# Optimization experiments

Measured on AMD Instinct MI355X. Metric: run time of the kernel, lower is better.

Reference implementation:

```python
import jax, jax.numpy as jnp
import numpy as np

N, D = 16384, 16     # nodes (hits), node feature dim (= embedding dim, slice is full)
K = 64               # max_num_neighbors
MAX_RADIUS = 6.0     # kNN radius cut
PID_MAX = 5000


def setup_inputs() -> dict:
    key = jax.random.key(0)
    k1, k2 = jax.random.split(key)
    x = jax.random.normal(k1, (N, D), dtype=jnp.float32)
    particle_id = jax.random.randint(k2, (N,), 0, PID_MAX, dtype=jnp.int32)
    return {"x": x, "particle_id": particle_id}


def reference(x, particle_id):
    # ml is None and embedding_slice=(None,None) -> embedding features are x itself
    emb = x
    # knn_graph: squared pairwise distances, self-loops excluded (diag = +inf)
    sq = jnp.sum(emb * emb, axis=1)                       # [N]
    d2 = sq[:, None] + sq[None, :] - 2.0 * (emb @ emb.T)  # [N, N]
    diag = jnp.arange(N)
    d2 = d2.at[diag, diag].set(jnp.inf)
    _, nbr = jax.lax.top_k(-d2, K)                        # [N, K] nearest neighbor ids
    src = nbr.reshape(-1)                                 # edge_index[0]: neighbor (source)
    dst = jnp.repeat(jnp.arange(N, dtype=src.dtype), K)   # edge_index[1]: query node
    # radius filter: keep edges with dist < max_radius (fixed shape -> boolean mask)
    diff = x[src] - x[dst]                                # [N*K, D]
    dists = jnp.sqrt(jnp.maximum(jnp.sum(diff * diff, axis=1), 0.0))
    mask = dists < MAX_RADIUS                             # [N*K]
    # edge truth labels: same (nonzero) particle id on both ends
    y = (particle_id[src] == particle_id[dst]) & (particle_id[src] > 0) & mask
    # edge features: [x_src - x_dst, x_src + x_dst], zeroed on masked-out edges
    edge_features = jnp.concatenate([diff, x[src] + x[dst]], axis=1)
    edge_features = edge_features * mask[:, None].astype(x.dtype)
    edge_index = jnp.stack([src, dst])                    # [2, N*K]
    return x, edge_index, y.astype(jnp.int32), edge_features, mask
```

## Files before the change

kernel.cpp:

```cpp
#include <hip/hip_runtime.h>

#define NN 16384
#define DD 16
#define KK 64
#define QQ 4
#define TPB 256
#define NQW 16
#define HIST 1024
#define HISTW (HIST/2)
#define LIST_MAX 768
#define CAND_MAX 256

__device__ __forceinline__ float halving_sumsq16(const float* v) {
    float p[16];
#pragma unroll
    for (int d = 0; d < 16; ++d) p[d] = __fmul_rn(v[d], v[d]);
    float r8[8];
#pragma unroll
    for (int j = 0; j < 8; ++j) r8[j] = __fadd_rn(p[j], p[j + 8]);
    float r4[4];
#pragma unroll
    for (int j = 0; j < 4; ++j) r4[j] = __fadd_rn(r8[j], r8[j + 4]);
    float r2[2];
#pragma unroll
    for (int j = 0; j < 2; ++j) r2[j] = __fadd_rn(r4[j], r4[j + 2]);
    return __fadd_rn(r2[0], r2[1]);
}

__device__ __forceinline__ float d2_of(const float* xi, const float* xj,
                                       float sqi, float sqj) {
    float dot = 0.0f;
#pragma unroll
    for (int d = 0; d < DD; ++d) dot = fmaf(xi[d], xj[d], dot);
    return __fsub_rn(__fadd_rn(sqi, sqj), __fmul_rn(2.0f, dot));
}

__device__ __forceinline__ int bucket_of(float d2) {
    int b = (int)__fmul_rn(d2, 4.0f);
    if (b < 0) b = 0;
    if (b >= HIST) b = HIST - 1;
    return b;
}

#define LOAD_XQ()                                                              \
    float xq[QQ][DD];                                                          \
    float sq[QQ], Tq[QQ];                                                      \
    _Pragma("unroll") for (int q = 0; q < QQ; ++q) {                           \
        const float4* p = reinterpret_cast<const float4*>(x + (iA + q) * DD);  \
        float4 a0 = p[0], a1 = p[1], a2 = p[2], a3 = p[3];                     \
        xq[q][0]=a0.x; xq[q][1]=a0.y; xq[q][2]=a0.z; xq[q][3]=a0.w;            \
        xq[q][4]=a1.x; xq[q][5]=a1.y; xq[q][6]=a1.z; xq[q][7]=a1.w;            \
        xq[q][8]=a2.x; xq[q][9]=a2.y; xq[q][10]=a2.z; xq[q][11]=a2.w;          \
        xq[q][12]=a3.x; xq[q][13]=a3.y; xq[q][14]=a3.z; xq[q][15]=a3.w;        \
        sq[q] = sqf[iA + q];                                                   \
        Tq[q] = 16.0f + sq[q] - 1.8f * sqrtf(32.0f + 4.0f * sq[q]);            \
    }

#define LOAD_XJ(j)                                                             \
    const float4* xj4 = reinterpret_cast<const float4*>(x + (j) * DD);         \
    float4 a0 = xj4[0], a1 = xj4[1], a2 = xj4[2], a3 = xj4[3];                 \
    float xj[DD] = {a0.x, a0.y, a0.z, a0.w, a1.x, a1.y, a1.z, a1.w,            \
                    a2.x, a2.y, a2.z, a2.w, a3.x, a3.y, a3.z, a3.w};

__global__ void prep_kernel(const float* __restrict__ x,
                            float* __restrict__ out_x,
                            float* __restrict__ sqf,
                            float* __restrict__ xt) {
    int i = blockIdx.x * blockDim.x + threadIdx.x;
    if (i < NN) {
        float v[DD];
#pragma unroll
        for (int d = 0; d < DD; ++d) v[d] = x[i * DD + d];
        sqf[i] = halving_sumsq16(v);
#pragma unroll
        for (int d = 0; d < DD; ++d) xt[d * NN + i] = v[d];
    }
    for (int t = i; t < NN * DD; t += gridDim.x * blockDim.x) {
        out_x[t] = x[t];
    }
}

__global__ __launch_bounds__(TPB, 6) void scan_kernel(
        const float* __restrict__ x,
        const float* __restrict__ xt,
        const float* __restrict__ sqf,
        unsigned int* __restrict__ ws_cnt,
        unsigned short* __restrict__ ws_list) {
    __shared__ unsigned short bm[NQW][TPB];
    __shared__ unsigned short list[QQ][LIST_MAX];
    __shared__ unsigned int wcnt[TPB / 64][QQ];
    __shared__ unsigned int s_listcnt[QQ];

    const int bid = blockIdx.x;
    const int tid = threadIdx.x;
    const int lane = tid & 63;
    const int w = tid >> 6;
    const int iA = bid * QQ;

    LOAD_XQ();

#pragma unroll 1
    for (int c = 0; c < NQW; ++c) {
        const int qd = c * TPB + tid;
        float4 sjv = reinterpret_cast<const float4*>(sqf)[qd];
        float4 acc[QQ];
#pragma unroll
        for (int q = 0; q < QQ; ++q) acc[q] = make_float4(0.f, 0.f, 0.f, 0.f);
#pragma unroll
        for (int d = 0; d < DD; ++d) {
            float4 xv = reinterpret_cast<const float4*>(xt + (long)d * NN)[qd];
#pragma unroll
            for (int q = 0; q < QQ; ++q) {
                acc[q].x = fmaf(xq[q][d], xv.x, acc[q].x);
                acc[q].y = fmaf(xq[q][d], xv.y, acc[q].y);
                acc[q].z = fmaf(xq[q][d], xv.z, acc[q].z);
                acc[q].w = fmaf(xq[q][d], xv.w, acc[q].w);
            }
        }
        unsigned int bits = 0;
#pragma unroll
        for (int q = 0; q < QQ; ++q) {
            float d2x = __fsub_rn(__fadd_rn(sq[q], sjv.x), __fmul_rn(2.0f, acc[q].x));
            float d2y = __fsub_rn(__fadd_rn(sq[q], sjv.y), __fmul_rn(2.0f, acc[q].y));
            float d2z = __fsub_rn(__fadd_rn(sq[q], sjv.z), __fmul_rn(2.0f, acc[q].z));
            float d2w = __fsub_rn(__fadd_rn(sq[q], sjv.w), __fmul_rn(2.0f, acc[q].w));
            if (d2x < Tq[q]) bits |= (1u << (0 * 4 + q));
            if (d2y < Tq[q]) bits |= (1u << (1 * 4 + q));
            if (d2z < Tq[q]) bits |= (1u << (2 * 4 + q));
            if (d2w < Tq[q]) bits |= (1u << (3 * 4 + q));
        }
        bm[c][tid] = (unsigned short)bits;
    }
    __syncthreads();

    {
        unsigned int cnt[QQ] = {0, 0, 0, 0};
#pragma unroll 1
        for (int c = 0; c < NQW; ++c) {
            unsigned int w16 = bm[c][tid];
#pragma unroll
            for (int q = 0; q < QQ; ++q)
                cnt[q] += (unsigned int)__popc(w16 & (0x1111u << q));
        }
        unsigned int excl[QQ];
#pragma unroll
        for (int q = 0; q < QQ; ++q) {
            unsigned int v = cnt[q];
#pragma unroll
            for (int off = 1; off < 64; off <<= 1) {
                unsigned int n = __shfl_up(v, off, 64);
                if (lane >= off) v += n;
            }
            excl[q] = v - cnt[q];
            if (lane == 63) wcnt[w][q] = v;
        }
        __syncthreads();
        if (tid < QQ)
            s_listcnt[tid] = wcnt[0][tid] + wcnt[1][tid] + wcnt[2][tid] + wcnt[3][tid];
        unsigned int cur[QQ];
#pragma unroll
        for (int q = 0; q < QQ; ++q) {
            unsigned int b = 0;
            for (int ww = 0; ww < w; ++ww) b += wcnt[ww][q];
            cur[q] = b + excl[q];
        }
#pragma unroll 1
        for (int c = 0; c < NQW; ++c) {
            unsigned int t16 = bm[c][tid];
            while (t16) {
                int b = __ffs(t16) - 1;
                int q = b & 3;
                int jl = b >> 2;
                unsigned int pos = cur[q]++;
                if (pos < LIST_MAX)
                    list[q][pos] = (unsigned short)((c * TPB + tid) * 4 + jl);
                t16 &= t16 - 1;
            }
        }
    }
    __syncthreads();

    for (int q = 0; q < QQ; ++q) {
        int lc = (int)min(s_listcnt[q], (unsigned int)LIST_MAX);
        unsigned short* dst = ws_list + ((long)iA + q) * LIST_MAX;
        for (int e = tid; e < lc; e += TPB) dst[e] = list[q][e];
    }
    if (tid < QQ) ws_cnt[iA + tid] = s_listcnt[tid];
}

__global__ __launch_bounds__(TPB) void select_kernel(
        const float* __restrict__ x,
        const int* __restrict__ pid,
        const float* __restrict__ sqf,
        const unsigned int* __restrict__ ws_cnt,
        const unsigned short* __restrict__ ws_list,
        float* __restrict__ out_src,
        float* __restrict__ out_dst,
        float* __restrict__ out_y,
        float* __restrict__ out_ef,
        float* __restrict__ out_mask) {
    __shared__ unsigned short list[QQ][LIST_MAX];
    __shared__ unsigned int hist[QQ][HISTW];
    __shared__ unsigned int cand_key[QQ][CAND_MAX];
    __shared__ int cand_idx[QQ][CAND_MAX];
    __shared__ unsigned int wavesum[QQ][TPB / 64];
    __shared__ int s_bsel[QQ];
    __shared__ unsigned int s_excnt[QQ], s_candcnt[QQ], s_lc[QQ];
    __shared__ int s_fb[QQ];

    const int bid = blockIdx.x;
    const int tid = threadIdx.x;
    const int lane = tid & 63;
    const int w = tid >> 6;
    const int iA = bid * QQ;

    for (int t = tid; t < QQ * HISTW; t += TPB)
        ((unsigned int*)hist)[t] = 0;
    if (tid < QQ) {
        s_excnt[tid] = 0; s_candcnt[tid] = 0; s_bsel[tid] = HIST - 1;
        s_lc[tid] = min(ws_cnt[iA + tid], (unsigned int)LIST_MAX);
    }
    LOAD_XQ();
    __syncthreads();

    for (int q = 0; q < QQ; ++q) {
        const unsigned short* src = ws_list + ((long)iA + q) * LIST_MAX;
        const int lc = (int)s_lc[q];
        for (int e = tid; e < lc; e += TPB) list[q][e] = src[e];
    }
    __syncthreads();

    for (int q = 0; q < QQ; ++q) {
        const int lc = (int)s_lc[q];
        unsigned int my = 0;
        for (int e = tid; e < lc; e += TPB) {
            const int j = list[q][e];
            LOAD_XJ(j);
            float d2 = d2_of(xq[q], xj, sq[q], sqf[j]);
            my += (d2 < Tq[q]) ? 1u : 0u;
            int b = bucket_of(d2);
            atomicAdd(&hist[q][b >> 1], 1u << ((b & 1) << 4));
        }
        unsigned int v = my;
#pragma unroll
        for (int off = 1; off < 64; off <<= 1) v += __shfl_xor(v, off, 64);
        if (lane == 0 && v) atomicAdd(&s_excnt[q], v);
    }
    __syncthreads();

    if (tid < QQ)
        s_fb[tid] = (ws_cnt[iA + tid] > LIST_MAX) || (s_excnt[tid] < KK + 1);
    __syncthreads();
    const int anyfb = s_fb[0] | s_fb[1] | s_fb[2] | s_fb[3];

    if (anyfb) {
#pragma unroll
        for (int q = 0; q < QQ; ++q)
            if (s_fb[q])
                for (int t = tid; t < HISTW; t += TPB) hist[q][t] = 0;
        __syncthreads();
        for (int j = tid; j < NN; j += TPB) {
            LOAD_XJ(j);
            const float sj = sqf[j];
#pragma unroll
            for (int q = 0; q < QQ; ++q) {
                if (s_fb[q] && j != iA + q) {
                    float d2 = d2_of(xq[q], xj, sq[q], sj);
                    int b = bucket_of(d2);
                    atomicAdd(&hist[q][b >> 1], 1u << ((b & 1) << 4));
                }
            }
        }
    }
    __syncthreads();

    {
        unsigned int local[QQ], inc[QQ];
        unsigned int pc0[QQ], pc1[QQ], pc2[QQ], pc3[QQ];
#pragma unroll
        for (int q = 0; q < QQ; ++q) {
            unsigned int h0 = hist[q][2 * tid];
            unsigned int h1 = hist[q][2 * tid + 1];
            pc0[q] = h0 & 0xFFFFu; pc1[q] = h0 >> 16;
            pc2[q] = h1 & 0xFFFFu; pc3[q] = h1 >> 16;
            unsigned int s = pc0[q] + pc1[q] + pc2[q] + pc3[q];
            local[q] = s;
            unsigned int v = s;
#pragma unroll
            for (int off = 1; off < 64; off <<= 1) {
                unsigned int n = __shfl_up(v, off, 64);
                if (lane >= off) v += n;
            }
            inc[q] = v;
        }
        if (lane == 63)
#pragma unroll
            for (int q = 0; q < QQ; ++q) wavesum[q][w] = inc[q];
        __syncthreads();
#pragma unroll
        for (int q = 0; q < QQ; ++q) {
            const unsigned int need = s_fb[q] ? KK : (KK + 1);
            unsigned int woff = 0;
            for (int ww = 0; ww < w; ++ww) woff += wavesum[q][ww];
            unsigned int cum = inc[q] + woff;
            unsigned int prev = cum - local[q];
            if (prev < need && need <= cum) {
                unsigned int acc = prev;
                int b = 4 * tid;
                if (acc + pc0[q] < need) { acc += pc0[q]; ++b;
                    if (acc + pc1[q] < need) { acc += pc1[q]; ++b;
                        if (acc + pc2[q] < need) { acc += pc2[q]; ++b; } } }
                s_bsel[q] = b;
            }
        }
    }
    __syncthreads();

#pragma unroll
    for (int q = 0; q < QQ; ++q) {
        if (!s_fb[q]) {
            const int bsel = s_bsel[q];
            const int lc = (int)s_lc[q];
            for (int e = tid; e < lc; e += TPB) {
                const int j = list[q][e];
                LOAD_XJ(j);
                float d2 = d2_of(xq[q], xj, sq[q], sqf[j]);
                if (bucket_of(d2) <= bsel && j != iA + q) {
                    unsigned int pos = atomicAdd(&s_candcnt[q], 1u);
                    if (pos < CAND_MAX) {
                        unsigned int u = __float_as_uint(d2);
                        u ^= (u & 0x80000000u) ? 0xFFFFFFFFu : 0x80000000u;
                        cand_key[q][pos] = u;
                        cand_idx[q][pos] = j;
                    }
                }
            }
        }
    }
    if (anyfb) {
        for (int j = tid; j < NN; j += TPB) {
            LOAD_XJ(j);
            const float sj = sqf[j];
#pragma unroll
            for (int q = 0; q < QQ; ++q) {
                if (s_fb[q] && j != iA + q) {
                    float d2 = d2_of(xq[q], xj, sq[q], sj);
                    if (bucket_of(d2) <= s_bsel[q]) {
                        unsigned int pos = atomicAdd(&s_candcnt[q], 1u);
                        if (pos < CAND_MAX) {
                            unsigned int u = __float_as_uint(d2);
                            u ^= (u & 0x80000000u) ? 0xFFFFFFFFu : 0x80000000u;
                            cand_key[q][pos] = u;
                            cand_idx[q][pos] = j;
                        }
                    }
                }
            }
        }
    }
    __syncthreads();

    for (int q = 0; q < QQ; ++q) {
        const int iq = iA + q;
        const int mypid = pid[iq];
        int c = (int)s_candcnt[q];
        if (c > CAND_MAX) c = CAND_MAX;
        for (int t = tid; t < c; t += TPB) {
            const unsigned int kt = cand_key[q][t];
            const int jt = cand_idx[q][t];
            int rank = 0;
            for (int u = 0; u < c; ++u) {
                unsigned int ku = cand_key[q][u];
                rank += (ku < kt) || (ku == kt && cand_idx[q][u] < jt);
            }
            if (rank < KK) {
                const long e = (long)iq * KK + rank;
                out_src[e] = (float)jt;

                const float* xjp = x + jt * DD;
                float diff[DD], sum[DD];
#pragma unroll
                for (int d = 0; d < DD; ++d) {
                    float a = xjp[d], b = xq[q][d];
                    diff[d] = __fsub_rn(a, b);
                    sum[d]  = __fadd_rn(a, b);
                }
                const float s2 = halving_sumsq16(diff);
                const bool m = __fsqrt_rn(s2) < 6.0f;
                out_mask[e] = m ? 1.0f : 0.0f;
                const int pj = pid[jt];
                out_y[e] = (m && pj == mypid && pj > 0) ? 1.0f : 0.0f;

                float* ef = out_ef + e * (2 * DD);
#pragma unroll
                for (int d = 0; d < DD; ++d) ef[d] = m ? diff[d] : 0.0f;
#pragma unroll
                for (int d = 0; d < DD; ++d) ef[DD + d] = m ? sum[d] : 0.0f;
            }
        }
    }

    for (int t = tid; t < QQ * KK; t += TPB) {
        out_dst[(long)iA * KK + t] = (float)(iA + t / KK);
    }
}

extern "C" void kernel_launch(void* const* d_in, const int* in_sizes, int n_in,
                              void* d_out, int out_size, void* d_ws, size_t ws_size,
                              hipStream_t stream) {
    const float* x = (const float*)d_in[0];
    const int* pid = (const int*)d_in[1];
    float* out = (float*)d_out;

    float* out_x   = out;
    float* out_src = out_x + NN * DD;
    float* out_dst = out_src + NN * KK;
    float* out_y   = out_dst + NN * KK;
    float* out_ef  = out_y + NN * KK;
    float* out_mask = out_ef + (long)NN * KK * 2 * DD;

    char* wsb = (char*)d_ws;
    float* sqf = (float*)wsb;
    float* xt = (float*)(wsb + (long)NN * 4);
    unsigned int* ws_cnt = (unsigned int*)(wsb + (long)NN * 4 + (long)NN * DD * 4);
    unsigned short* ws_list =
        (unsigned short*)(wsb + (long)NN * 4 + (long)NN * DD * 4 + (long)NN * 4);

    prep_kernel<<<NN / 256, 256, 0, stream>>>(x, out_x, sqf, xt);
    scan_kernel<<<NN / QQ, TPB, 0, stream>>>(x, xt, sqf, ws_cnt, ws_list);
    select_kernel<<<NN / QQ, TPB, 0, stream>>>(x, pid, sqf, ws_cnt, ws_list,
                                               out_src, out_dst, out_y,
                                               out_ef, out_mask);
}
```

Baseline: 374.9 us.

## Use packed fp16 dot products in candidate scan with widened threshold

Stores x in a transposed packed half2 layout and computes the candidate-filter dot products with packed fp16 FMAs instead of fp32, halving the bytes loaded and the FMA instruction count in the scan. To absorb fp16 error, the candidate threshold is loosened (coefficient 1.8 to 2.0, plus an EPS margin) and the comparison is rewritten as dot > sj/2 + C. Exact distances are still recomputed later in fp32. The looser threshold may admit more candidates, which could overflow list limits or add selection work. Launch bounds occupancy is lowered from 6 to 4.

```diff
diff --git a/kernel.cpp b/kernel.cpp
--- a/kernel.cpp
+++ b/kernel.cpp
@@ -1,4 +1,5 @@
 #include <hip/hip_runtime.h>
+#include <hip/hip_fp16.h>
 
 #define NN 16384
 #define DD 16
@@ -10,6 +11,7 @@
 #define HISTW (HIST/2)
 #define LIST_MAX 768
 #define CAND_MAX 256
+#define EPS 1.5f
 
 __device__ __forceinline__ float halving_sumsq16(const float* v) {
     float p[16];
@@ -40,6 +42,10 @@
     if (b < 0) b = 0;
     if (b >= HIST) b = HIST - 1;
     return b;
+}
+
+__device__ __forceinline__ float tq_of(float s) {
+    return 16.0f + s - 2.0f * sqrtf(32.0f + 4.0f * s);
 }
 
 #define LOAD_XQ()                                                              \
@@ -53,7 +59,7 @@
         xq[q][8]=a2.x; xq[q][9]=a2.y; xq[q][10]=a2.z; xq[q][11]=a2.w;          \
         xq[q][12]=a3.x; xq[q][13]=a3.y; xq[q][14]=a3.z; xq[q][15]=a3.w;        \
         sq[q] = sqf[iA + q];                                                   \
-        Tq[q] = 16.0f + sq[q] - 1.8f * sqrtf(32.0f + 4.0f * sq[q]);            \
+        Tq[q] = tq_of(sq[q]);                                                  \
     }
 
 #define LOAD_XJ(j)                                                             \
@@ -65,7 +71,7 @@
 __global__ void prep_kernel(const float* __restrict__ x,
                             float* __restrict__ out_x,
                             float* __restrict__ sqf,
-                            float* __restrict__ xt) {
+                            __half* __restrict__ xh) {
     int i = blockIdx.x * blockDim.x + threadIdx.x;
     if (i < NN) {
         float v[DD];
@@ -73,16 +79,18 @@
         for (int d = 0; d < DD; ++d) v[d] = x[i * DD + d];
         sqf[i] = halving_sumsq16(v);
 #pragma unroll
-        for (int d = 0; d < DD; ++d) xt[d * NN + i] = v[d];
+        for (int p = 0; p < 8; ++p) {
+            xh[((long)p * NN + i) * 2 + 0] = __float2half(v[2 * p]);
+            xh[((long)p * NN + i) * 2 + 1] = __float2half(v[2 * p + 1]);
+        }
     }
     for (int t = i; t < NN * DD; t += gridDim.x * blockDim.x) {
         out_x[t] = x[t];
     }
 }
 
-__global__ __launch_bounds__(TPB, 6) void scan_kernel(
-        const float* __restrict__ x,
-        const float* __restrict__ xt,
+__global__ __launch_bounds__(TPB, 4) void scan_kernel(
+        const __half2* __restrict__ xh2,
         const float* __restrict__ sqf,
         unsigned int* __restrict__ ws_cnt,
         unsigned short* __restrict__ ws_list) {
@@ -91,43 +99,60 @@
     __shared__ unsigned int wcnt[TPB / 64][QQ];
     __shared__ unsigned int s_listcnt[QQ];
 
-    const int bid = blockIdx.x;
     const int tid = threadIdx.x;
     const int lane = tid & 63;
     const int w = tid >> 6;
-    const int iA = bid * QQ;
-
-    LOAD_XQ();
+    const int iA = blockIdx.x * QQ;
+
+    __half2 qh[QQ][8];
+    float Cq[QQ];
+#pragma unroll
+    for (int q = 0; q < QQ; ++q) {
+        const float* xr = (const float*)sqf;
+    }
+#pragma unroll
+    for (int q = 0; q < QQ; ++q)
+#pragma unroll
+        for (int p = 0; p < 8; ++p)
+            qh[q][p] = xh2[(long)p * NN + (iA + q)];
+#pragma unroll
+    for (int q = 0; q < QQ; ++q) {
+        float s = sqf[iA + q];
+        Cq[q] = 0.5f * (s - tq_of(s) - EPS);
+    }
 
 #pragma unroll 1
     for (int c = 0; c < NQW; ++c) {
         const int qd = c * TPB + tid;
         float4 sjv = reinterpret_cast<const float4*>(sqf)[qd];
-        float4 acc[QQ];
-#pragma unroll
-        for (int q = 0; q < QQ; ++q) acc[q] = make_float4(0.f, 0.f, 0.f, 0.f);
-#pragma unroll
-        for (int d = 0; d < DD; ++d) {
-            float4 xv = reinterpret_cast<const float4*>(xt + (long)d * NN)[qd];
+        __half2 acc[QQ][4];
+#pragma unroll
+        for (int q = 0; q < QQ; ++q)
+#pragma unroll
+            for (int jl = 0; jl < 4; ++jl)
+                acc[q][jl] = __half2(__float2half(0.f), __float2half(0.f));
+#pragma unroll
+        for (int p = 0; p < 8; ++p) {
+            const __half2* hp = &xh2[(long)p * NN + 4 * (long)qd];
+            __half2 h0 = hp[0], h1 = hp[1], h2 = hp[2], h3 = hp[3];
 #pragma unroll
             for (int q = 0; q < QQ; ++q) {
-                acc[q].x = fmaf(xq[q][d], xv.x, acc[q].x);
-                acc[q].y = fmaf(xq[q][d], xv.y, acc[q].y);
-                acc[q].z = fmaf(xq[q][d], xv.z, acc[q].z);
-                acc[q].w = fmaf(xq[q][d], xv.w, acc[q].w);
+                acc[q][0] = __hfma2(qh[q][p], h0, acc[q][0]);
+                acc[q][1] = __hfma2(qh[q][p], h1, acc[q][1]);
+                acc[q][2] = __hfma2(qh[q][p], h2, acc[q][2]);
+                acc[q][3] = __hfma2(qh[q][p], h3, acc[q][3]);
             }
         }
         unsigned int bits = 0;
-#pragma unroll
-        for (int q = 0; q < QQ; ++q) {
-            float d2x = __fsub_rn(__fadd_rn(sq[q], sjv.x), __fmul_rn(2.0f, acc[q].x));
-            float d2y = __fsub_rn(__fadd_rn(sq[q], sjv.y), __fmul_rn(2.0f, acc[q].y));
-            float d2z = __fsub_rn(__fadd_rn(sq[q], sjv.z), __fmul_rn(2.0f, acc[q].z));
-            float d2w = __fsub_rn(__fadd_rn(sq[q], sjv.w), __fmul_rn(2.0f, acc[q].w));
-            if (d2x < Tq[q]) bits |= (1u << (0 * 4 + q));
-            if (d2y < Tq[q]) bits |= (1u << (1 * 4 + q));
-            if (d2z < Tq[q]) bits |= (1u << (2 * 4 + q));
-            if (d2w < Tq[q]) bits |= (1u << (3 * 4 + q));
+        float sjq[4] = {sjv.x, sjv.y, sjv.z, sjv.w};
+#pragma unroll
+        for (int jl = 0; jl < 4; ++jl) {
+#pragma unroll
+            for (int q = 0; q < QQ; ++q) {
+                float dot = __low2float(acc[q][jl]) + __high2float(acc[q][jl]);
+                float thr = fmaf(sjq[jl], 0.5f, Cq[q]);
+                if (dot > thr) bits |= (1u << (jl * 4 + q));
+            }
         }
         bm[c][tid] = (unsigned short)bits;
     }
@@ -421,13 +446,15 @@
 
     char* wsb = (char*)d_ws;
     float* sqf = (float*)wsb;
-    float* xt = (float*)(wsb + (long)NN * 4);
-    unsigned int* ws_cnt = (unsigned int*)(wsb + (long)NN * 4 + (long)NN * DD * 4);
+    __half* xh = (__half*)(wsb + (long)NN * 4);
+    unsigned int* ws_cnt =
+        (unsigned int*)(wsb + (long)NN * 4 + (long)NN * DD * 2);
     unsigned short* ws_list =
-        (unsigned short*)(wsb + (long)NN * 4 + (long)NN * DD * 4 + (long)NN * 4);
-
-    prep_kernel<<<NN / 256, 256, 0, stream>>>(x, out_x, sqf, xt);
-    scan_kernel<<<NN / QQ, TPB, 0, stream>>>(x, xt, sqf, ws_cnt, ws_list);
+        (unsigned short*)(wsb + (long)NN * 4 + (long)NN * DD * 2 + (long)NN * 4);
+
+    prep_kernel<<<NN / 256, 256, 0, stream>>>(x, out_x, sqf, xh);
+    scan_kernel<<<NN / QQ, TPB, 0, stream>>>((const __half2*)xh, sqf,
+                                             ws_cnt, ws_list);
     select_kernel<<<NN / QQ, TPB, 0, stream>>>(x, pid, sqf, ws_cnt, ws_list,
                                                out_src, out_dst, out_y,
                                                out_ef, out_mask);
```

Result: slower. 418.9 us (+11.7%).
